# Kernel tuning notes

Measured on AMD Instinct MI355X. Metric: run time of the kernel, lower is better.

Reference implementation:

```python
import jax, jax.numpy as jnp
import numpy as np

# Production YOLOv3 head decode config (finest FPN scale, fpn_idx=2)
B = 32            # batch
A = 3             # box_per_anchor
NC = 80           # n_classes (COCO)
ATTR = 5 + NC     # objness, x, y, w, h, class confidences
GH = GW = 76      # grid size = 608 // 8
IN_W = IN_H = 608 # network input resolution


def setup_inputs() -> dict:
    key = jax.random.key(0)
    k1, k2 = jax.random.split(key)
    # scale down so exp(tw), exp(th) stay in a realistic range
    features = jax.random.normal(k1, (B, A * ATTR, GH, GW), dtype=jnp.float32) * 0.5
    # canonical YOLOv3 small-object anchors: (10,13),(16,30),(33,23) flattened
    anchor_size = jnp.array([10.0, 13.0, 16.0, 30.0, 33.0, 23.0], dtype=jnp.float32)
    return {"features": features, "anchor_size": anchor_size}


def reference(features, anchor_size):
    """Vectorized equivalent of DarkNet53.transform_grid_data.

    features:    [B, A*ATTR, GH, GW] raw head outputs
    anchor_size: [2*A] flat (w, h) anchor pairs for this FPN scale
    returns:     [B, A*GH*GW, ATTR] decoded boxes, row layout
                 [objness, box_x, box_y, box_w, box_h, class_conf...]
                 with rows ordered (anchor b, row j, col i) to match the
                 original nested-loop stacking order.
    """
    Bn, C, gh, gw = features.shape
    wpg = IN_W // gw  # width_per_grid (stride)
    hpg = IN_H // gh  # height_per_grid

    f = features.reshape(Bn, A, ATTR, gh, gw)

    obj = jax.nn.sigmoid(f[:, :, 0])  # [B,A,gh,gw]
    xs = jnp.arange(gw, dtype=features.dtype)
    ys = jnp.arange(gh, dtype=features.dtype)
    box_x = (jax.nn.sigmoid(f[:, :, 1]) + xs[None, None, None, :]) * wpg
    box_y = (jax.nn.sigmoid(f[:, :, 2]) + ys[None, None, :, None]) * hpg

    aw = anchor_size[0::2][None, :, None, None]  # [1,A,1,1]
    ah = anchor_size[1::2][None, :, None, None]
    box_w = aw * jnp.exp(f[:, :, 3]) * wpg
    box_h = ah * jnp.exp(f[:, :, 4]) * hpg

    conf = f[:, :, 5:]  # raw class scores (original applies no sigmoid here)

    head = jnp.stack([obj, box_x, box_y, box_w, box_h], axis=2)  # [B,A,5,gh,gw]
    out = jnp.concatenate([head, conf], axis=2)                  # [B,A,ATTR,gh,gw]
    # -> [B, A, gh, gw, ATTR] -> [B, A*gh*gw, ATTR], matching loop order (b, j, i)
    out = jnp.transpose(out, (0, 1, 3, 4, 2)).reshape(Bn, A * gh * gw, ATTR)
    return out
```

## Files before the change

### kernel.cpp

```cpp
#include <hip/hip_runtime.h>


#define A_    3
#define ATTR_ 85
#define GW_   76
#define SP_   (76 * 76)
#define TS    64
#define NT    256

typedef float f32x4 __attribute__((ext_vector_type(4)));

__global__ __launch_bounds__(NT) void darknet_decode_kernel(
    const float* __restrict__ in,
    const float* __restrict__ anchors,
    float* __restrict__ out) {

    const int tile  = blockIdx.x;
    const int plane = blockIdx.y;
    const int a     = plane % A_;

    const int s0 = tile * TS;
    const int ns = (SP_ - s0 < TS) ? (SP_ - s0) : TS;

    __shared__ float lds[TS * ATTR_];

    const float aw = anchors[2 * a]     * 8.0f;
    const float ah = anchors[2 * a + 1] * 8.0f;

    const float* __restrict__ inp = in + (size_t)plane * (ATTR_ * SP_) + s0;

    const int tx4   = threadIdx.x & 15;
    const int ty    = threadIdx.x >> 4;
    const int sbase = 4 * tx4;

    if (sbase < ns) {
        f32x4 v[6];
        #pragma unroll
        for (int it = 0; it < 5; ++it) {
            v[it] = *reinterpret_cast<const f32x4*>(inp + (size_t)(ty + 16 * it) * SP_ + sbase);
        }
        const bool six = (ty < 5);
        if (six) {
            v[5] = *reinterpret_cast<const f32x4*>(inp + (size_t)(80 + ty) * SP_ + sbase);
        }

        if (ty < 5) {
            #pragma unroll
            for (int k = 0; k < 4; ++k) {
                const int s = s0 + sbase + k;
                const float x = v[0][k];
                float r;
                if (ty == 0)      r = 1.0f / (1.0f + __expf(-x));
                else if (ty == 1) r = (1.0f / (1.0f + __expf(-x)) + (float)(s % GW_)) * 8.0f;
                else if (ty == 2) r = (1.0f / (1.0f + __expf(-x)) + (float)(s / GW_)) * 8.0f;
                else if (ty == 3) r = aw * __expf(x);
                else              r = ah * __expf(x);
                v[0][k] = r;
            }
        }

        #pragma unroll
        for (int it = 0; it < 5; ++it) {
            const int attr = ty + 16 * it;
            #pragma unroll
            for (int k = 0; k < 4; ++k)
                lds[(sbase + k) * ATTR_ + attr] = v[it][k];
        }
        if (six) {
            const int attr = 80 + ty;
            #pragma unroll
            for (int k = 0; k < 4; ++k)
                lds[(sbase + k) * ATTR_ + attr] = v[5][k];
        }
    }
    __syncthreads();

    float* __restrict__ outp = out + (size_t)plane * ((size_t)SP_ * ATTR_) + (size_t)s0 * ATTR_;
    const int nf4 = (ns * ATTR_) >> 2;
    const f32x4* __restrict__ lds4 = reinterpret_cast<const f32x4*>(lds);
    f32x4* __restrict__ out4 = reinterpret_cast<f32x4*>(outp);

    f32x4 w[6];
    #pragma unroll
    for (int it = 0; it < 6; ++it) {
        const int idx = (int)threadIdx.x + NT * it;
        if (idx < nf4) w[it] = lds4[idx];
    }
    #pragma unroll
    for (int it = 0; it < 6; ++it) {
        const int idx = (int)threadIdx.x + NT * it;
        if (idx < nf4) __builtin_nontemporal_store(w[it], &out4[idx]);
    }
}

extern "C" void kernel_launch(void* const* d_in, const int* in_sizes, int n_in,
                              void* d_out, int out_size, void* d_ws, size_t ws_size,
                              hipStream_t stream) {
    const float* features = (const float*)d_in[0];
    const float* anchors  = (const float*)d_in[1];
    float* out = (float*)d_out;

    const int tiles_per_plane = (SP_ + TS - 1) / TS;
    const int planes = 32 * A_;
    dim3 grid(tiles_per_plane, planes);
    darknet_decode_kernel<<<grid, NT, 0, stream>>>(features, anchors, out);
}
```

Baseline: 66.11 us.

## Make each wave transpose its own 16-position chunks without block barriers

Each of the block's four waves now owns its own LDS slice and processes two 16-position chunks independently. It transposes the channel-major input to row-major output through wave-private LDS, so the block-wide __syncthreads is gone. The aim is to let waves stream loads and stores without waiting on each other. In exchange, each global read per channel row shrinks to a 64-byte segment, which may coalesce less well than the earlier 256-byte rows, and each wave handles its two chunks one after the other.

```diff
diff --git a/kernel.cpp b/kernel.cpp
--- a/kernel.cpp
+++ b/kernel.cpp
@@ -1,12 +1,14 @@
 #include <hip/hip_runtime.h>
 
 
-#define A_    3
-#define ATTR_ 85
-#define GW_   76
-#define SP_   (76 * 76)
-#define TS    64
-#define NT    256
+#define A_     3
+#define ATTR_  85
+#define GW_    76
+#define SP_    (76 * 76)
+#define NCHUNK 361
+#define WAVES  4
+#define CPW    2
+#define NT     256
 
 typedef float f32x4 __attribute__((ext_vector_type(4)));
 
@@ -15,81 +17,82 @@
     const float* __restrict__ anchors,
     float* __restrict__ out) {
 
-    const int tile  = blockIdx.x;
     const int plane = blockIdx.y;
     const int a     = plane % A_;
+    const int wv    = threadIdx.x >> 6;
+    const int l     = threadIdx.x & 63;
+    const int al    = l >> 2;
+    const int pq    = l & 3;
 
-    const int s0 = tile * TS;
-    const int ns = (SP_ - s0 < TS) ? (SP_ - s0) : TS;
-
-    __shared__ float lds[TS * ATTR_];
+    __shared__ float lds[WAVES * 16 * ATTR_];
+    float* __restrict__ wl = lds + wv * (16 * ATTR_);
 
     const float aw = anchors[2 * a]     * 8.0f;
     const float ah = anchors[2 * a + 1] * 8.0f;
 
-    const float* __restrict__ inp = in + (size_t)plane * (ATTR_ * SP_) + s0;
+    const float* __restrict__ inp = in + (size_t)plane * ((size_t)ATTR_ * SP_);
+    const int c0 = blockIdx.x * (WAVES * CPW) + wv * CPW;
 
-    const int tx4   = threadIdx.x & 15;
-    const int ty    = threadIdx.x >> 4;
-    const int sbase = 4 * tx4;
-
-    if (sbase < ns) {
-        f32x4 v[6];
-        #pragma unroll
-        for (int it = 0; it < 5; ++it) {
-            v[it] = *reinterpret_cast<const f32x4*>(inp + (size_t)(ty + 16 * it) * SP_ + sbase);
-        }
-        const bool six = (ty < 5);
-        if (six) {
-            v[5] = *reinterpret_cast<const f32x4*>(inp + (size_t)(80 + ty) * SP_ + sbase);
-        }
-
-        if (ty < 5) {
+    f32x4 v[CPW][6];
+    #pragma unroll
+    for (int j = 0; j < CPW; ++j) {
+        const int c = c0 + j;
+        if (c < NCHUNK) {
+            const float* p = inp + c * 16 + 4 * pq;
             #pragma unroll
-            for (int k = 0; k < 4; ++k) {
-                const int s = s0 + sbase + k;
-                const float x = v[0][k];
-                float r;
-                if (ty == 0)      r = 1.0f / (1.0f + __expf(-x));
-                else if (ty == 1) r = (1.0f / (1.0f + __expf(-x)) + (float)(s % GW_)) * 8.0f;
-                else if (ty == 2) r = (1.0f / (1.0f + __expf(-x)) + (float)(s / GW_)) * 8.0f;
-                else if (ty == 3) r = aw * __expf(x);
-                else              r = ah * __expf(x);
-                v[0][k] = r;
-            }
-        }
-
-        #pragma unroll
-        for (int it = 0; it < 5; ++it) {
-            const int attr = ty + 16 * it;
-            #pragma unroll
-            for (int k = 0; k < 4; ++k)
-                lds[(sbase + k) * ATTR_ + attr] = v[it][k];
-        }
-        if (six) {
-            const int attr = 80 + ty;
-            #pragma unroll
-            for (int k = 0; k < 4; ++k)
-                lds[(sbase + k) * ATTR_ + attr] = v[5][k];
+            for (int it = 0; it < 5; ++it)
+                v[j][it] = *reinterpret_cast<const f32x4*>(p + (size_t)(16 * it + al) * SP_);
+            if (al < 5)
+                v[j][5] = *reinterpret_cast<const f32x4*>(p + (size_t)(80 + al) * SP_);
         }
     }
-    __syncthreads();
 
-    float* __restrict__ outp = out + (size_t)plane * ((size_t)SP_ * ATTR_) + (size_t)s0 * ATTR_;
-    const int nf4 = (ns * ATTR_) >> 2;
-    const f32x4* __restrict__ lds4 = reinterpret_cast<const f32x4*>(lds);
-    f32x4* __restrict__ out4 = reinterpret_cast<f32x4*>(outp);
+    #pragma unroll
+    for (int j = 0; j < CPW; ++j) {
+        const int c = c0 + j;
+        if (c < NCHUNK) {
+            if (al < 5) {
+                #pragma unroll
+                for (int k = 0; k < 4; ++k) {
+                    const int s = c * 16 + 4 * pq + k;
+                    const float x = v[j][0][k];
+                    float r;
+                    if (al == 0)      r = 1.0f / (1.0f + __expf(-x));
+                    else if (al == 1) r = (1.0f / (1.0f + __expf(-x)) + (float)(s % GW_)) * 8.0f;
+                    else if (al == 2) r = (1.0f / (1.0f + __expf(-x)) + (float)(s / GW_)) * 8.0f;
+                    else if (al == 3) r = aw * __expf(x);
+                    else              r = ah * __expf(x);
+                    v[j][0][k] = r;
+                }
+            }
 
-    f32x4 w[6];
-    #pragma unroll
-    for (int it = 0; it < 6; ++it) {
-        const int idx = (int)threadIdx.x + NT * it;
-        if (idx < nf4) w[it] = lds4[idx];
-    }
-    #pragma unroll
-    for (int it = 0; it < 6; ++it) {
-        const int idx = (int)threadIdx.x + NT * it;
-        if (idx < nf4) __builtin_nontemporal_store(w[it], &out4[idx]);
+            #pragma unroll
+            for (int it = 0; it < 5; ++it) {
+                const int attr = 16 * it + al;
+                #pragma unroll
+                for (int k = 0; k < 4; ++k)
+                    wl[(4 * pq + k) * ATTR_ + attr] = v[j][it][k];
+            }
+            if (al < 5) {
+                const int attr = 80 + al;
+                #pragma unroll
+                for (int k = 0; k < 4; ++k)
+                    wl[(4 * pq + k) * ATTR_ + attr] = v[j][5][k];
+            }
+
+            const f32x4* __restrict__ wl4 = reinterpret_cast<const f32x4*>(wl);
+            f32x4* __restrict__ op4 = reinterpret_cast<f32x4*>(
+                out + ((size_t)plane * SP_ + (size_t)c * 16) * ATTR_);
+            f32x4 t[6];
+            #pragma unroll
+            for (int it = 0; it < 5; ++it) t[it] = wl4[l + 64 * it];
+            if (l < 20) t[5] = wl4[l + 320];
+            #pragma unroll
+            for (int it = 0; it < 5; ++it)
+                __builtin_nontemporal_store(t[it], &op4[l + 64 * it]);
+            if (l < 20)
+                __builtin_nontemporal_store(t[5], &op4[l + 320]);
+        }
     }
 }
 
@@ -100,8 +103,8 @@
     const float* anchors  = (const float*)d_in[1];
     float* out = (float*)d_out;
 
-    const int tiles_per_plane = (SP_ + TS - 1) / TS;
-    const int planes = 32 * A_;
-    dim3 grid(tiles_per_plane, planes);
+    const int chunks_per_block = WAVES * CPW;
+    const int bx = (NCHUNK + chunks_per_block - 1) / chunks_per_block;
+    dim3 grid(bx, 32 * A_);
     darknet_decode_kernel<<<grid, NT, 0, stream>>>(features, anchors, out);
 }
```

Result: no change. 65.64 us, median of 2 (-0.7%).
